# Performance work log

Hardware: AMD Instinct MI355X
Metric: run time of the kernel (lower is better)

The kernel has to match this reference:

```python
import jax, jax.numpy as jnp
import numpy as np

NUM_CLASSES = 2
NORM_EPS = 1e-12   # F.normalize default
COS_EPS = 1e-8     # nn.CosineSimilarity default
MEAN_EPS = 1e-6


def _l2_normalize_c(x):
    # normalize over channel dim (dim=1), per (batch, pixel) -- matches
    # F.normalize(x.view(-1,16,256*256), dim=1)
    n = jnp.sqrt(jnp.sum(x * x, axis=1, keepdims=True))
    return x / jnp.maximum(n, NORM_EPS)


def _cos_c(a, b):
    # cosine similarity along channel dim, torch semantics
    dot = jnp.sum(a * b, axis=1)
    na = jnp.sqrt(jnp.sum(a * a, axis=1))
    nb = jnp.sqrt(jnp.sum(b * b, axis=1))
    return dot / jnp.maximum(na * nb, COS_EPS)


def setup_inputs() -> dict:
    key = jax.random.key(0)
    k1, k2, k3 = jax.random.split(key, 3)
    preds_S = jax.random.normal(k1, (32, 16, 256, 256), dtype=jnp.float32)
    preds_T = jax.random.normal(k2, (32, 16, 256, 256), dtype=jnp.float32)
    target = jax.random.randint(k3, (32, 256, 256), 0, NUM_CLASSES, dtype=jnp.int64)
    return {"preds_S": preds_S, "preds_T": preds_T, "target": target}


def reference(preds_S, preds_T, target):
    feat_S = _l2_normalize_c(preds_S)  # [B,16,H,W]
    feat_T = _l2_normalize_c(preds_T)
    # target is already HxW == feature size, so nearest upsample is identity
    tar = target[:, None, :, :].astype(feat_S.dtype)  # [B,1,H,W], broadcasts over C

    center_S, center_T = feat_S, feat_T
    center_S_FS, center_T_FS = feat_S, feat_T
    for i in range(NUM_CLASSES):
        mask = (tar == i).astype(feat_S.dtype)  # [B,1,H,W]
        cnt = jnp.sum(mask, axis=(-2, -1)) + MEAN_EPS  # [B,1]
        mean_S = (jnp.sum(mask * feat_S, axis=(-2, -1)) / cnt)[:, :, None, None]  # [B,16,1,1]
        mean_T = (jnp.sum(mask * feat_T, axis=(-2, -1)) / cnt)[:, :, None, None]
        center_S = (1.0 - mask) * center_S + mask * mean_S
        center_T = (1.0 - mask) * center_T + mask * mean_T
        center_S_FS = mask * center_S_FS + (1.0 - mask) * mean_S
        center_T_FS = mask * center_T_FS + (1.0 - mask) * mean_T

    pcsim_S = jnp.exp(_cos_c(feat_S, center_S) - _cos_c(feat_S, center_S_FS))
    pcsim_T = jnp.exp(_cos_c(feat_T, center_T) - _cos_c(feat_T, center_T_FS))
    return jnp.mean((pcsim_S - pcsim_T) ** 2)
```

## Files before the change

kernel.cpp:

```cpp
#include <hip/hip_runtime.h>
#include <math.h>

#define NBATCH 32
#define NCH 16
#define HW 65536
#define SLICES1 32
#define SLICES2 32
#define TPB 256
#define NBLK2 (SLICES2 * NBATCH)

#define WS_PART  0
#define WS_N1P   65536
#define WS_LOSSP 66560
#define WS_CNT   67584
#define WS_FLOATS 67600

__device__ __forceinline__ float wave_sum(float v) {
#pragma unroll
  for (int off = 32; off > 0; off >>= 1) v += __shfl_down(v, off, 64);
  return v;
}

__global__ __launch_bounds__(TPB) void k_sums(const float* __restrict__ S,
                                              const float* __restrict__ T,
                                              const int* __restrict__ tgt,
                                              float* __restrict__ ws) {
  const int b = blockIdx.y;
  const int slice = blockIdx.x;
  const int which = blockIdx.z;
  const int tid = threadIdx.x;
  const int lane = tid & 63, wid = tid >> 6;

  if (slice == 0 && b == 0 && which == 0 && tid == 0)
    *reinterpret_cast<int*>(ws + WS_CNT) = 0;

  const float* Xb = (which ? T : S) + (size_t)b * NCH * HW;
  const int* tb = tgt + (size_t)b * HW;

  const int base = slice * (HW / SLICES1) + tid * 4;

  float acc0[NCH], acc1[NCH];
#pragma unroll
  for (int i = 0; i < NCH; ++i) { acc0[i] = 0.f; acc1[i] = 0.f; }
  float n1 = 0.f;

  for (int it = 0; it < 2; ++it) {
    const int p = base + it * (TPB * 4);
    const int4 tv = *(const int4*)(tb + p);
    float4 x[NCH];
#pragma unroll
    for (int i = 0; i < NCH; ++i)
      x[i] = *(const float4*)(Xb + (size_t)i * HW + p);

    const float m0 = (tv.x == 1) ? 1.f : 0.f;
    const float m1 = (tv.y == 1) ? 1.f : 0.f;
    const float m2 = (tv.z == 1) ? 1.f : 0.f;
    const float m3 = (tv.w == 1) ? 1.f : 0.f;
    n1 += (m0 + m1) + (m2 + m3);

    float s0a = 0.f, s0b = 0.f, s1a = 0.f, s1b = 0.f;
    float s2a = 0.f, s2b = 0.f, s3a = 0.f, s3b = 0.f;
#pragma unroll
    for (int i = 0; i < NCH; i += 2) {
      s0a = fmaf(x[i].x, x[i].x, s0a);   s0b = fmaf(x[i + 1].x, x[i + 1].x, s0b);
      s1a = fmaf(x[i].y, x[i].y, s1a);   s1b = fmaf(x[i + 1].y, x[i + 1].y, s1b);
      s2a = fmaf(x[i].z, x[i].z, s2a);   s2b = fmaf(x[i + 1].z, x[i + 1].z, s2b);
      s3a = fmaf(x[i].w, x[i].w, s3a);   s3b = fmaf(x[i + 1].w, x[i + 1].w, s3b);
    }
    const float i0 = 1.f / fmaxf(sqrtf(s0a + s0b), 1e-12f);
    const float i1 = 1.f / fmaxf(sqrtf(s1a + s1b), 1e-12f);
    const float i2 = 1.f / fmaxf(sqrtf(s2a + s2b), 1e-12f);
    const float i3 = 1.f / fmaxf(sqrtf(s3a + s3b), 1e-12f);

#pragma unroll
    for (int i = 0; i < NCH; ++i) {
      const float f0 = x[i].x * i0, f1 = x[i].y * i1;
      const float f2 = x[i].z * i2, f3 = x[i].w * i3;
      const float t_ = (f0 + f1) + (f2 + f3);
      const float m_ = fmaf(f0, m0, fmaf(f1, m1, fmaf(f2, m2, f3 * m3)));
      acc1[i] += m_;
      acc0[i] += t_ - m_;
    }
  }

  __shared__ float lds[32][TPB + 1];
  __shared__ float redn[4];
#pragma unroll
  for (int i = 0; i < NCH; ++i) {
    lds[i][tid] = acc0[i];
    lds[16 + i][tid] = acc1[i];
  }
  n1 = wave_sum(n1);
  if (lane == 0) redn[wid] = n1;
  __syncthreads();

  const int row = tid >> 3, seg = tid & 7;
  float s = 0.f;
#pragma unroll
  for (int k0 = 0; k0 < 32; ++k0) {
    const int k = (k0 + seg * 4) & 31;
    s += lds[row][seg * 32 + k];
  }
  s += __shfl_down(s, 4, 8);
  s += __shfl_down(s, 2, 8);
  s += __shfl_down(s, 1, 8);

  float* part = ws + WS_PART + (((size_t)which * NBATCH + b) * SLICES1 + slice) * 32;
  if (seg == 0) part[row] = s;
  if (tid == 0 && which == 0)
    ws[WS_N1P + b * SLICES1 + slice] = redn[0] + redn[1] + redn[2] + redn[3];
}

__device__ __forceinline__ float pc_one(float ss, float d0, float d1, int t,
                                        float nm0, float nm1) {
  const float n = sqrtf(ss);
  const float inv = 1.f / fmaxf(n, 1e-12f);
  const float na = n * inv;
  const float c0 = (d0 * inv) / fmaxf(na * nm0, 1e-8f);
  const float c1 = (d1 * inv) / fmaxf(na * nm1, 1e-8f);
  return expf((t == 1) ? (c1 - c0) : (c0 - c1));
}

__global__ __launch_bounds__(TPB) void k_pass2(const float* __restrict__ S,
                                               const float* __restrict__ T,
                                               const int* __restrict__ tgt,
                                               float* __restrict__ ws,
                                               float* __restrict__ out) {
  __shared__ __align__(16) float sm[72];
  __shared__ float ldp[4][64];
  __shared__ float ldn[32];
  __shared__ float red4[4];
  __shared__ int isLast;
  const int b = blockIdx.y;
  const int slice = blockIdx.x;
  const int tid = threadIdx.x;

  {
    const int c64 = tid & 63, q = tid >> 6;
    const int t_ = c64 >> 5, c32 = c64 & 31;
    const float* pp = ws + WS_PART + (((size_t)t_ * NBATCH + b) * SLICES1) * 32 + c32;
    float s8 = 0.f;
#pragma unroll
    for (int k = 0; k < 8; ++k) s8 += pp[(q * 8 + k) * 32];
    ldp[q][c64] = s8;
  }
  if (tid < 32) ldn[tid] = ws[WS_N1P + b * SLICES1 + tid];
  __syncthreads();

  if (tid < 64) {
    float n1 = 0.f;
#pragma unroll
    for (int k = 0; k < 32; ++k) n1 += ldn[k];
    const int cls = (tid >> 4) & 1;
    const float cnt = (cls ? n1 : ((float)HW - n1)) + 1e-6f;
    sm[tid] = (ldp[0][tid] + ldp[1][tid] + ldp[2][tid] + ldp[3][tid]) / cnt;
  }
  __syncthreads();
  if (tid < 4) {
    float ss = 0.f;
    const int base_ = (tid >> 1) * 32 + (tid & 1) * 16;
#pragma unroll
    for (int c = 0; c < NCH; ++c) { const float v = sm[base_ + c]; ss = fmaf(v, v, ss); }
    sm[64 + tid] = sqrtf(ss);
  }
  __syncthreads();

  const int base = slice * (HW / SLICES2) + tid * 2;
  const float* Sb = S + (size_t)b * NCH * HW;
  const float* Tb = T + (size_t)b * NCH * HW;
  const int* tb = tgt + (size_t)b * HW;

  const float nmS0 = sm[64], nmS1 = sm[65], nmT0 = sm[66], nmT1 = sm[67];
  float lacc = 0.f;

  for (int it = 0; it < 4; ++it) {
    const int p = base + it * (TPB * 2);
    const int2 tv = *(const int2*)(tb + p);
    float2 xs[NCH], xt[NCH];
#pragma unroll
    for (int i = 0; i < NCH; ++i)
      xs[i] = *(const float2*)(Sb + (size_t)i * HW + p);
#pragma unroll
    for (int i = 0; i < NCH; ++i)
      xt[i] = *(const float2*)(Tb + (size_t)i * HW + p);

    float ss0 = 0.f, ss1 = 0.f, d00 = 0.f, d01 = 0.f, d10 = 0.f, d11 = 0.f;
#pragma unroll
    for (int i = 0; i < NCH; ++i) {
      const float w0 = sm[i], w1 = sm[16 + i];
      ss0 = fmaf(xs[i].x, xs[i].x, ss0); ss1 = fmaf(xs[i].y, xs[i].y, ss1);
      d00 = fmaf(xs[i].x, w0, d00);      d01 = fmaf(xs[i].y, w0, d01);
      d10 = fmaf(xs[i].x, w1, d10);      d11 = fmaf(xs[i].y, w1, d11);
    }
    const float pcS0 = pc_one(ss0, d00, d10, tv.x, nmS0, nmS1);
    const float pcS1 = pc_one(ss1, d01, d11, tv.y, nmS0, nmS1);

    ss0 = 0.f; ss1 = 0.f; d00 = 0.f; d01 = 0.f; d10 = 0.f; d11 = 0.f;
#pragma unroll
    for (int i = 0; i < NCH; ++i) {
      const float w0 = sm[32 + i], w1 = sm[48 + i];
      ss0 = fmaf(xt[i].x, xt[i].x, ss0); ss1 = fmaf(xt[i].y, xt[i].y, ss1);
      d00 = fmaf(xt[i].x, w0, d00);      d01 = fmaf(xt[i].y, w0, d01);
      d10 = fmaf(xt[i].x, w1, d10);      d11 = fmaf(xt[i].y, w1, d11);
    }
    const float pcT0 = pc_one(ss0, d00, d10, tv.x, nmT0, nmT1);
    const float pcT1 = pc_one(ss1, d01, d11, tv.y, nmT0, nmT1);

    const float e0 = pcS0 - pcT0, e1 = pcS1 - pcT1;
    lacc += e0 * e0 + e1 * e1;
  }

  lacc = wave_sum(lacc);
  if ((tid & 63) == 0) red4[tid >> 6] = lacc;
  __syncthreads();

  const int bidx = b * SLICES2 + slice;
  if (tid == 0) {
    ws[WS_LOSSP + bidx] = red4[0] + red4[1] + red4[2] + red4[3];
    __threadfence();
    const int old = atomicAdd(reinterpret_cast<int*>(ws + WS_CNT), 1);
    isLast = (old == NBLK2 - 1);
  }
  __syncthreads();

  if (isLast) {
    __threadfence();
    if (tid < 64) {
      float s = 0.f;
#pragma unroll
      for (int k = 0; k < NBLK2 / 64; ++k) s += ws[WS_LOSSP + tid + 64 * k];
      s = wave_sum(s);
      if (tid == 0) out[0] = s * (1.f / 2097152.f);
    }
  }
}

extern "C" void kernel_launch(void* const* d_in, const int* in_sizes, int n_in,
                              void* d_out, int out_size, void* d_ws, size_t ws_size,
                              hipStream_t stream) {
  const float* S = (const float*)d_in[0];
  const float* T = (const float*)d_in[1];
  const int* tgt = (const int*)d_in[2];
  float* ws = (float*)d_ws;
  float* out = (float*)d_out;

  dim3 g1(SLICES1, NBATCH, 2);
  k_sums<<<g1, TPB, 0, stream>>>(S, T, tgt, ws);
  dim3 g2(SLICES2, NBATCH);
  k_pass2<<<g2, TPB, 0, stream>>>(S, T, tgt, ws, out);
}
```

Measured before the change: 364.6 us.

## Cache normalized features in fp16 workspace for second pass

```diff
diff --git a/kernel.cpp b/kernel.cpp
--- a/kernel.cpp
+++ b/kernel.cpp
@@ -7,13 +7,17 @@
 #define SLICES1 32
 #define SLICES2 32
 #define TPB 256
-#define NBLK2 (SLICES2 * NBATCH)
-
-#define WS_PART  0
-#define WS_N1P   65536
-#define WS_LOSSP 66560
-#define WS_CNT   67584
-#define WS_FLOATS 67600
+
+#define CT_PART  0
+#define CT_N1P   65536
+#define CT_LOSSP 66560
+#define CT_FLOATS 67584
+
+#define CACHE_HALFS ((size_t)2 * NBATCH * NCH * HW)
+#define CACHE_BYTES (CACHE_HALFS * 2)
+
+typedef float f4 __attribute__((ext_vector_type(4)));
+typedef _Float16 h4 __attribute__((ext_vector_type(4)));
 
 __device__ __forceinline__ float wave_sum(float v) {
 #pragma unroll
@@ -21,21 +25,21 @@
   return v;
 }
 
+template <bool CACHE>
 __global__ __launch_bounds__(TPB) void k_sums(const float* __restrict__ S,
                                               const float* __restrict__ T,
                                               const int* __restrict__ tgt,
-                                              float* __restrict__ ws) {
+                                              float* __restrict__ ctrl,
+                                              _Float16* __restrict__ cache) {
   const int b = blockIdx.y;
   const int slice = blockIdx.x;
   const int which = blockIdx.z;
   const int tid = threadIdx.x;
   const int lane = tid & 63, wid = tid >> 6;
 
-  if (slice == 0 && b == 0 && which == 0 && tid == 0)
-    *reinterpret_cast<int*>(ws + WS_CNT) = 0;
-
   const float* Xb = (which ? T : S) + (size_t)b * NCH * HW;
   const int* tb = tgt + (size_t)b * HW;
+  _Float16* cb = cache + ((size_t)(which * NBATCH + b)) * NCH * HW;
 
   const int base = slice * (HW / SLICES1) + tid * 4;
 
@@ -47,10 +51,10 @@
   for (int it = 0; it < 2; ++it) {
     const int p = base + it * (TPB * 4);
     const int4 tv = *(const int4*)(tb + p);
-    float4 x[NCH];
+    f4 x[NCH];
 #pragma unroll
     for (int i = 0; i < NCH; ++i)
-      x[i] = *(const float4*)(Xb + (size_t)i * HW + p);
+      x[i] = __builtin_nontemporal_load((const f4*)(Xb + (size_t)i * HW + p));
 
     const float m0 = (tv.x == 1) ? 1.f : 0.f;
     const float m1 = (tv.y == 1) ? 1.f : 0.f;
@@ -76,6 +80,12 @@
     for (int i = 0; i < NCH; ++i) {
       const float f0 = x[i].x * i0, f1 = x[i].y * i1;
       const float f2 = x[i].z * i2, f3 = x[i].w * i3;
+      if constexpr (CACHE) {
+        h4 q;
+        q.x = (_Float16)f0; q.y = (_Float16)f1;
+        q.z = (_Float16)f2; q.w = (_Float16)f3;
+        __builtin_nontemporal_store(q, (h4*)(cb + (size_t)i * HW + p));
+      }
       const float t_ = (f0 + f1) + (f2 + f3);
       const float m_ = fmaf(f0, m0, fmaf(f1, m1, fmaf(f2, m2, f3 * m3)));
       acc1[i] += m_;
@@ -105,10 +115,10 @@
   s += __shfl_down(s, 2, 8);
   s += __shfl_down(s, 1, 8);
 
-  float* part = ws + WS_PART + (((size_t)which * NBATCH + b) * SLICES1 + slice) * 32;
+  float* part = ctrl + CT_PART + (((size_t)which * NBATCH + b) * SLICES1 + slice) * 32;
   if (seg == 0) part[row] = s;
   if (tid == 0 && which == 0)
-    ws[WS_N1P + b * SLICES1 + slice] = redn[0] + redn[1] + redn[2] + redn[3];
+    ctrl[CT_N1P + b * SLICES1 + slice] = redn[0] + redn[1] + redn[2] + redn[3];
 }
 
 __device__ __forceinline__ float pc_one(float ss, float d0, float d1, int t,
@@ -121,16 +131,16 @@
   return expf((t == 1) ? (c1 - c0) : (c0 - c1));
 }
 
+template <bool CACHE>
 __global__ __launch_bounds__(TPB) void k_pass2(const float* __restrict__ S,
                                                const float* __restrict__ T,
                                                const int* __restrict__ tgt,
-                                               float* __restrict__ ws,
-                                               float* __restrict__ out) {
+                                               float* __restrict__ ctrl,
+                                               const _Float16* __restrict__ cache) {
   __shared__ __align__(16) float sm[72];
   __shared__ float ldp[4][64];
   __shared__ float ldn[32];
   __shared__ float red4[4];
-  __shared__ int isLast;
   const int b = blockIdx.y;
   const int slice = blockIdx.x;
   const int tid = threadIdx.x;
@@ -138,13 +148,13 @@
   {
     const int c64 = tid & 63, q = tid >> 6;
     const int t_ = c64 >> 5, c32 = c64 & 31;
-    const float* pp = ws + WS_PART + (((size_t)t_ * NBATCH + b) * SLICES1) * 32 + c32;
+    const float* pp = ctrl + CT_PART + (((size_t)t_ * NBATCH + b) * SLICES1) * 32 + c32;
     float s8 = 0.f;
 #pragma unroll
     for (int k = 0; k < 8; ++k) s8 += pp[(q * 8 + k) * 32];
     ldp[q][c64] = s8;
   }
-  if (tid < 32) ldn[tid] = ws[WS_N1P + b * SLICES1 + tid];
+  if (tid < 32) ldn[tid] = ctrl[CT_N1P + b * SLICES1 + tid];
   __syncthreads();
 
   if (tid < 64) {
@@ -165,74 +175,124 @@
   }
   __syncthreads();
 
-  const int base = slice * (HW / SLICES2) + tid * 2;
-  const float* Sb = S + (size_t)b * NCH * HW;
-  const float* Tb = T + (size_t)b * NCH * HW;
   const int* tb = tgt + (size_t)b * HW;
-
-  const float nmS0 = sm[64], nmS1 = sm[65], nmT0 = sm[66], nmT1 = sm[67];
   float lacc = 0.f;
 
-  for (int it = 0; it < 4; ++it) {
-    const int p = base + it * (TPB * 2);
-    const int2 tv = *(const int2*)(tb + p);
-    float2 xs[NCH], xt[NCH];
-#pragma unroll
-    for (int i = 0; i < NCH; ++i)
-      xs[i] = *(const float2*)(Sb + (size_t)i * HW + p);
-#pragma unroll
-    for (int i = 0; i < NCH; ++i)
-      xt[i] = *(const float2*)(Tb + (size_t)i * HW + p);
-
-    float ss0 = 0.f, ss1 = 0.f, d00 = 0.f, d01 = 0.f, d10 = 0.f, d11 = 0.f;
-#pragma unroll
-    for (int i = 0; i < NCH; ++i) {
-      const float w0 = sm[i], w1 = sm[16 + i];
-      ss0 = fmaf(xs[i].x, xs[i].x, ss0); ss1 = fmaf(xs[i].y, xs[i].y, ss1);
-      d00 = fmaf(xs[i].x, w0, d00);      d01 = fmaf(xs[i].y, w0, d01);
-      d10 = fmaf(xs[i].x, w1, d10);      d11 = fmaf(xs[i].y, w1, d11);
+  if constexpr (CACHE) {
+    const _Float16* cS = cache + (size_t)b * NCH * HW;
+    const _Float16* cT = cache + ((size_t)(NBATCH + b)) * NCH * HW;
+    const float rS0 = 1.f / fmaxf(sm[64], 1e-8f);
+    const float rS1 = 1.f / fmaxf(sm[65], 1e-8f);
+    const float rT0 = 1.f / fmaxf(sm[66], 1e-8f);
+    const float rT1 = 1.f / fmaxf(sm[67], 1e-8f);
+    const int base = slice * (HW / SLICES2) + tid * 4;
+
+    for (int it = 0; it < 2; ++it) {
+      const int p = base + it * (TPB * 4);
+      const int4 tv = *(const int4*)(tb + p);
+      h4 xs[NCH], xt[NCH];
+#pragma unroll
+      for (int i = 0; i < NCH; ++i)
+        xs[i] = __builtin_nontemporal_load((const h4*)(cS + (size_t)i * HW + p));
+#pragma unroll
+      for (int i = 0; i < NCH; ++i)
+        xt[i] = __builtin_nontemporal_load((const h4*)(cT + (size_t)i * HW + p));
+
+      f4 a0 = {0, 0, 0, 0}, a1 = {0, 0, 0, 0};
+#pragma unroll
+      for (int i = 0; i < NCH; ++i) {
+        const float w0 = sm[i], w1 = sm[16 + i];
+        const float x0 = (float)xs[i].x, x1 = (float)xs[i].y;
+        const float x2 = (float)xs[i].z, x3 = (float)xs[i].w;
+        a0.x = fmaf(x0, w0, a0.x); a0.y = fmaf(x1, w0, a0.y);
+        a0.z = fmaf(x2, w0, a0.z); a0.w = fmaf(x3, w0, a0.w);
+        a1.x = fmaf(x0, w1, a1.x); a1.y = fmaf(x1, w1, a1.y);
+        a1.z = fmaf(x2, w1, a1.z); a1.w = fmaf(x3, w1, a1.w);
+      }
+      const float pcS0 = expf((tv.x == 1) ? a1.x * rS1 - a0.x * rS0 : a0.x * rS0 - a1.x * rS1);
+      const float pcS1 = expf((tv.y == 1) ? a1.y * rS1 - a0.y * rS0 : a0.y * rS0 - a1.y * rS1);
+      const float pcS2 = expf((tv.z == 1) ? a1.z * rS1 - a0.z * rS0 : a0.z * rS0 - a1.z * rS1);
+      const float pcS3 = expf((tv.w == 1) ? a1.w * rS1 - a0.w * rS0 : a0.w * rS0 - a1.w * rS1);
+
+      a0 = {0, 0, 0, 0}; a1 = {0, 0, 0, 0};
+#pragma unroll
+      for (int i = 0; i < NCH; ++i) {
+        const float w0 = sm[32 + i], w1 = sm[48 + i];
+        const float x0 = (float)xt[i].x, x1 = (float)xt[i].y;
+        const float x2 = (float)xt[i].z, x3 = (float)xt[i].w;
+        a0.x = fmaf(x0, w0, a0.x); a0.y = fmaf(x1, w0, a0.y);
+        a0.z = fmaf(x2, w0, a0.z); a0.w = fmaf(x3, w0, a0.w);
+        a1.x = fmaf(x0, w1, a1.x); a1.y = fmaf(x1, w1, a1.y);
+        a1.z = fmaf(x2, w1, a1.z); a1.w = fmaf(x3, w1, a1.w);
+      }
+      const float pcT0 = expf((tv.x == 1) ? a1.x * rT1 - a0.x * rT0 : a0.x * rT0 - a1.x * rT1);
+      const float pcT1 = expf((tv.y == 1) ? a1.y * rT1 - a0.y * rT0 : a0.y * rT0 - a1.y * rT1);
+      const float pcT2 = expf((tv.z == 1) ? a1.z * rT1 - a0.z * rT0 : a0.z * rT0 - a1.z * rT1);
+      const float pcT3 = expf((tv.w == 1) ? a1.w * rT1 - a0.w * rT0 : a0.w * rT0 - a1.w * rT1);
+
+      const float e0 = pcS0 - pcT0, e1 = pcS1 - pcT1;
+      const float e2 = pcS2 - pcT2, e3 = pcS3 - pcT3;
+      lacc += (e0 * e0 + e1 * e1) + (e2 * e2 + e3 * e3);
     }
-    const float pcS0 = pc_one(ss0, d00, d10, tv.x, nmS0, nmS1);
-    const float pcS1 = pc_one(ss1, d01, d11, tv.y, nmS0, nmS1);
-
-    ss0 = 0.f; ss1 = 0.f; d00 = 0.f; d01 = 0.f; d10 = 0.f; d11 = 0.f;
-#pragma unroll
-    for (int i = 0; i < NCH; ++i) {
-      const float w0 = sm[32 + i], w1 = sm[48 + i];
-      ss0 = fmaf(xt[i].x, xt[i].x, ss0); ss1 = fmaf(xt[i].y, xt[i].y, ss1);
-      d00 = fmaf(xt[i].x, w0, d00);      d01 = fmaf(xt[i].y, w0, d01);
-      d10 = fmaf(xt[i].x, w1, d10);      d11 = fmaf(xt[i].y, w1, d11);
+  } else {
+    const float* Sb = S + (size_t)b * NCH * HW;
+    const float* Tb = T + (size_t)b * NCH * HW;
+    const float nmS0 = sm[64], nmS1 = sm[65], nmT0 = sm[66], nmT1 = sm[67];
+    const int base = slice * (HW / SLICES2) + tid * 2;
+
+    for (int it = 0; it < 4; ++it) {
+      const int p = base + it * (TPB * 2);
+      const int2 tv = *(const int2*)(tb + p);
+      float2 xs[NCH], xt[NCH];
+#pragma unroll
+      for (int i = 0; i < NCH; ++i) xs[i] = *(const float2*)(Sb + (size_t)i * HW + p);
+#pragma unroll
+      for (int i = 0; i < NCH; ++i) xt[i] = *(const float2*)(Tb + (size_t)i * HW + p);
+
+      float ss0 = 0.f, ss1 = 0.f, d00 = 0.f, d01 = 0.f, d10 = 0.f, d11 = 0.f;
+#pragma unroll
+      for (int i = 0; i < NCH; ++i) {
+        const float w0 = sm[i], w1 = sm[16 + i];
+        ss0 = fmaf(xs[i].x, xs[i].x, ss0); ss1 = fmaf(xs[i].y, xs[i].y, ss1);
+        d00 = fmaf(xs[i].x, w0, d00);      d01 = fmaf(xs[i].y, w0, d01);
+        d10 = fmaf(xs[i].x, w1, d10);      d11 = fmaf(xs[i].y, w1, d11);
+      }
+      const float pcS0 = pc_one(ss0, d00, d10, tv.x, nmS0, nmS1);
+      const float pcS1 = pc_one(ss1, d01, d11, tv.y, nmS0, nmS1);
+
+      ss0 = 0.f; ss1 = 0.f; d00 = 0.f; d01 = 0.f; d10 = 0.f; d11 = 0.f;
+#pragma unroll
+      for (int i = 0; i < NCH; ++i) {
+        const float w0 = sm[32 + i], w1 = sm[48 + i];
+        ss0 = fmaf(xt[i].x, xt[i].x, ss0); ss1 = fmaf(xt[i].y, xt[i].y, ss1);
+        d00 = fmaf(xt[i].x, w0, d00);      d01 = fmaf(xt[i].y, w0, d01);
+        d10 = fmaf(xt[i].x, w1, d10);      d11 = fmaf(xt[i].y, w1, d11);
+      }
+      const float pcT0 = pc_one(ss0, d00, d10, tv.x, nmT0, nmT1);
+      const float pcT1 = pc_one(ss1, d01, d11, tv.y, nmT0, nmT1);
+
+      const float e0 = pcS0 - pcT0, e1 = pcS1 - pcT1;
+      lacc += e0 * e0 + e1 * e1;
     }
-    const float pcT0 = pc_one(ss0, d00, d10, tv.x, nmT0, nmT1);
-    const float pcT1 = pc_one(ss1, d01, d11, tv.y, nmT0, nmT1);
-
-    const float e0 = pcS0 - pcT0, e1 = pcS1 - pcT1;
-    lacc += e0 * e0 + e1 * e1;
   }
 
   lacc = wave_sum(lacc);
   if ((tid & 63) == 0) red4[tid >> 6] = lacc;
   __syncthreads();
-
-  const int bidx = b * SLICES2 + slice;
-  if (tid == 0) {
-    ws[WS_LOSSP + bidx] = red4[0] + red4[1] + red4[2] + red4[3];
-    __threadfence();
-    const int old = atomicAdd(reinterpret_cast<int*>(ws + WS_CNT), 1);
-    isLast = (old == NBLK2 - 1);
-  }
-  __syncthreads();
-
-  if (isLast) {
-    __threadfence();
-    if (tid < 64) {
-      float s = 0.f;
-#pragma unroll
-      for (int k = 0; k < NBLK2 / 64; ++k) s += ws[WS_LOSSP + tid + 64 * k];
-      s = wave_sum(s);
-      if (tid == 0) out[0] = s * (1.f / 2097152.f);
-    }
-  }
+  if (tid == 0)
+    ctrl[CT_LOSSP + b * SLICES2 + slice] = red4[0] + red4[1] + red4[2] + red4[3];
+}
+
+__global__ void k_final(const float* __restrict__ ctrl, float* __restrict__ out) {
+  __shared__ float r4[4];
+  const int tid = threadIdx.x;
+  float s = ctrl[CT_LOSSP + tid] + ctrl[CT_LOSSP + tid + 256] +
+            ctrl[CT_LOSSP + tid + 512] + ctrl[CT_LOSSP + tid + 768];
+  s = wave_sum(s);
+  if ((tid & 63) == 0) r4[tid >> 6] = s;
+  __syncthreads();
+  if (tid == 0)
+    out[0] = (r4[0] + r4[1] + r4[2] + r4[3]) * (1.f / 2097152.f);
 }
 
 extern "C" void kernel_launch(void* const* d_in, const int* in_sizes, int n_in,
@@ -241,11 +301,21 @@
   const float* S = (const float*)d_in[0];
   const float* T = (const float*)d_in[1];
   const int* tgt = (const int*)d_in[2];
-  float* ws = (float*)d_ws;
   float* out = (float*)d_out;
 
+  const size_t need = CACHE_BYTES + (size_t)CT_FLOATS * 4;
+  const bool cached = ws_size >= need;
+  _Float16* cache = (_Float16*)d_ws;
+  float* ctrl = cached ? (float*)((char*)d_ws + CACHE_BYTES) : (float*)d_ws;
+
   dim3 g1(SLICES1, NBATCH, 2);
-  k_sums<<<g1, TPB, 0, stream>>>(S, T, tgt, ws);
   dim3 g2(SLICES2, NBATCH);
-  k_pass2<<<g2, TPB, 0, stream>>>(S, T, tgt, ws, out);
-}
+  if (cached) {
+    k_sums<true><<<g1, TPB, 0, stream>>>(S, T, tgt, ctrl, cache);
+    k_pass2<true><<<g2, TPB, 0, stream>>>(S, T, tgt, ctrl, cache);
+  } else {
+    k_sums<false><<<g1, TPB, 0, stream>>>(S, T, tgt, ctrl, cache);
+    k_pass2<false><<<g2, TPB, 0, stream>>>(S, T, tgt, ctrl, cache);
+  }
+  k_final<<<1, 256, 0, stream>>>(ctrl, out);
+}
```

New measurement: 316.2 us. 1.15x faster.
